# Optimization experiments

Hardware: AMD Instinct MI355X
Metric: run time of the kernel (lower is better)

Reference implementation:

```python
import jax, jax.numpy as jnp
import numpy as np

NUM_PRODUCTS = 100000
NUM_CATEGORIES = 1000
P_DIM = 64          # product embedding dim
C_DIM = P_DIM // 2  # 32
T_DIM = P_DIM // 4  # 16
U_DIM = P_DIM // 4  # 16
HID = 128
B, S, L = 1024, 50, 20


def setup_inputs() -> dict:
    key = jax.random.key(0)
    ks = jax.random.split(key, 24)
    inp = {}
    inp['product_input'] = jax.random.randint(ks[0], (B, S, L), 1, NUM_PRODUCTS + 1, dtype=jnp.int32)
    inp['categories_input'] = jax.random.randint(ks[1], (B, S, L), 1, NUM_CATEGORIES + 1, dtype=jnp.int32)
    inp['user_age_input'] = jax.random.uniform(ks[2], (B,), jnp.float32) * 80.0
    inp['user_timestamps_input'] = jax.random.uniform(ks[3], (B, S), jnp.float32)
    inp['user_gender_input'] = jax.random.randint(ks[4], (B,), 0, 2).astype(jnp.float32)
    # embedding tables (padding_idx=0 -> zero row)
    emb_p = jax.random.normal(ks[5], (NUM_PRODUCTS + 1, P_DIM), jnp.float32) * 0.02
    inp['emb_p'] = emb_p.at[0].set(0.0)
    emb_c = jax.random.normal(ks[6], (NUM_CATEGORIES + 1, C_DIM), jnp.float32) * 0.02
    inp['emb_c'] = emb_c.at[0].set(0.0)
    # small linears
    inp['W_ts'] = jax.random.normal(ks[7], (T_DIM, 1), jnp.float32) * 0.1
    inp['b_ts'] = jnp.zeros((T_DIM,), jnp.float32)
    inp['W_uf'] = jax.random.normal(ks[8], (U_DIM, 2), jnp.float32) * 0.1
    inp['b_uf'] = jnp.zeros((U_DIM,), jnp.float32)
    # 2-layer LSTM params (torch layout: [4H, in], gate order i,f,g,o)
    IN = P_DIM + C_DIM + T_DIM + U_DIM  # 128
    sc = 1.0 / np.sqrt(HID)
    inp['W_ih0'] = jax.random.uniform(ks[9], (4 * HID, IN), jnp.float32, -sc, sc)
    inp['W_hh0'] = jax.random.uniform(ks[10], (4 * HID, HID), jnp.float32, -sc, sc)
    inp['b_ih0'] = jax.random.uniform(ks[11], (4 * HID,), jnp.float32, -sc, sc)
    inp['b_hh0'] = jax.random.uniform(ks[12], (4 * HID,), jnp.float32, -sc, sc)
    inp['W_ih1'] = jax.random.uniform(ks[13], (4 * HID, HID), jnp.float32, -sc, sc)
    inp['W_hh1'] = jax.random.uniform(ks[14], (4 * HID, HID), jnp.float32, -sc, sc)
    inp['b_ih1'] = jax.random.uniform(ks[15], (4 * HID,), jnp.float32, -sc, sc)
    inp['b_hh1'] = jax.random.uniform(ks[16], (4 * HID,), jnp.float32, -sc, sc)
    # MLP head
    inp['W1'] = jax.random.normal(ks[17], (HID // 2, HID), jnp.float32) * 0.05
    inp['b1'] = jnp.zeros((HID // 2,), jnp.float32)
    inp['W2'] = jax.random.normal(ks[18], (NUM_PRODUCTS + 1, HID // 2), jnp.float32) * 0.05
    inp['b2'] = jnp.zeros((NUM_PRODUCTS + 1,), jnp.float32)
    return inp


def _lstm_layer(x, Wih, Whh, bih, bhh):
    # x: [S, B, D] -> outputs [S, B, H], final h [B, H]
    Bb = x.shape[1]
    h0 = jnp.zeros((Bb, HID), x.dtype)
    def step(carry, xt):
        h, c = carry
        gates = xt @ Wih.T + bih + h @ Whh.T + bhh
        i, f, g, o = jnp.split(gates, 4, axis=-1)
        c = jax.nn.sigmoid(f) * c + jax.nn.sigmoid(i) * jnp.tanh(g)
        h = jax.nn.sigmoid(o) * jnp.tanh(c)
        return (h, c), h
    (h, c), ys = jax.lax.scan(step, (h0, h0), x)
    return ys, h


def reference(product_input, categories_input, user_age_input, user_timestamps_input,
              user_gender_input, emb_p, emb_c, W_ts, b_ts, W_uf, b_uf,
              W_ih0, W_hh0, b_ih0, b_hh0, W_ih1, W_hh1, b_ih1, b_hh1,
              W1, b1, W2, b2):
    # per-basket mean-pooled embeddings (fused gather + segment mean)
    prod = emb_p[product_input].mean(axis=2)          # [B, S, 64]
    cat = emb_c[categories_input].mean(axis=2)        # [B, S, 32]
    ts = user_timestamps_input[..., None] @ W_ts.T + b_ts  # [B, S, 16]
    uf = jnp.stack([user_age_input, user_gender_input], axis=1) @ W_uf.T + b_uf  # [B, 16]
    uf = jnp.broadcast_to(uf[:, None, :], (uf.shape[0], prod.shape[1], uf.shape[1]))
    x = jnp.concatenate([prod, cat, ts, uf], axis=-1)  # [B, S, 128]
    x = jnp.transpose(x, (1, 0, 2))                    # [S, B, 128]
    ys0, _ = _lstm_layer(x, W_ih0, W_hh0, b_ih0, b_hh0)
    _, h_last = _lstm_layer(ys0, W_ih1, W_hh1, b_ih1, b_hh1)  # [B, H]
    # dropout is identity in eval mode
    hidden = jax.nn.relu(h_last @ W1.T + b1)
    logits = hidden @ W2.T + b2                        # [B, num_products+1]
    return logits
```

## Files before the change

kernel.cpp:

```cpp
#include <hip/hip_runtime.h>

#define B_    1024
#define S_    50
#define L_    20
#define NOUT  100001

typedef __attribute__((ext_vector_type(8))) short bh8;
typedef __attribute__((ext_vector_type(4))) float fx4;

__device__ __forceinline__ unsigned short f2bf(float x){
  unsigned u = __float_as_uint(x);
  unsigned r = (u + 0x7FFFu + ((u >> 16) & 1u)) >> 16;
  return (unsigned short)r;
}
__device__ __forceinline__ float bf2f(unsigned short h){
  return __uint_as_float(((unsigned)h) << 16);
}
__device__ __forceinline__ float sigm(float x){ return 1.f/(1.f + __expf(-x)); }
__device__ __forceinline__ float tanh_(float x){ return 1.f - 2.f/(__expf(2.f*x) + 1.f); }

__device__ __forceinline__ void frag_convert_row(const float* src, bh8& hv, bh8& lv){
  #pragma unroll
  for (int j = 0; j < 8; j++){
    float x = src[j];
    unsigned short hb = f2bf(x);
    hv[j] = (short)hb;
    lv[j] = (short)f2bf(x - bf2f(hb));
  }
}

__global__ __launch_bounds__(256) void prep_lstm_w(
    const float* __restrict__ Wih0, const float* __restrict__ Whh0,
    const float* __restrict__ bih0, const float* __restrict__ bhh0,
    const float* __restrict__ Wih1, const float* __restrict__ Whh1,
    const float* __restrict__ bih1, const float* __restrict__ bhh1,
    short* __restrict__ wsw, float* __restrict__ wsbias){
  int tid = blockIdx.x*256 + threadIdx.x;
  if (tid < 1024){
    int l = tid >> 9, n = tid & 511;
    wsbias[l*512 + n] = l ? (bih1[n] + bhh1[n]) : (bih0[n] + bhh0[n]);
  }
  if (tid >= 32768) return;
  int lane = tid & 63;
  int kt   = (tid >> 6) & 7;
  int nt   = (tid >> 9) & 31;
  int l    = tid >> 14;
  const float* Wih = l ? Wih1 : Wih0;
  const float* Whh = l ? Whh1 : Whh0;
  int n = nt*16 + (lane & 15);
  int kbase = kt*32 + (lane >> 4)*8;
  size_t base = ((((size_t)l*32 + nt)*8 + kt)*64 + lane)*8;
  for (int j = 0; j < 8; j++){
    int k = kbase + j;
    float w = (k < 128) ? Wih[n*128 + k] : Whh[n*128 + (k - 128)];
    wsw[base + j] = (short)f2bf(w);
  }
}

__global__ __launch_bounds__(256) void prep_w2(const float* __restrict__ W2,
                                               short* __restrict__ out){
  long i = (long)blockIdx.x*256 + threadIdx.x;
  if (i >= 100016L*64) return;
  long row = i >> 6;
  float v = (row < NOUT) ? W2[i] : 0.f;
  out[i] = (short)f2bf(v);
}

__global__ __launch_bounds__(256) void features(
    const int* __restrict__ pidx, const int* __restrict__ cidx,
    const float* __restrict__ age, const float* __restrict__ ts,
    const float* __restrict__ gender,
    const float* __restrict__ embp, const float* __restrict__ embc,
    const float* __restrict__ Wts, const float* __restrict__ bts,
    const float* __restrict__ Wuf, const float* __restrict__ bufv,
    short* __restrict__ xfrag){
  const int bx = blockIdx.x;
  const int bt = bx & 63, s = bx >> 6;
  const int b0 = bt*16;
  const int tid = threadIdx.x;
  __shared__ int pi[320], ci[320];
  __shared__ __align__(16) float XF[16][132];
  for (int i = tid; i < 640; i += 256){
    if (i < 320){
      int row = i/20, l = i - row*20;
      pi[i] = pidx[((size_t)(b0+row)*S_ + s)*L_ + l];
    } else {
      int j = i - 320;
      int row = j/20, l = j - row*20;
      ci[j] = cidx[((size_t)(b0+row)*S_ + s)*L_ + l];
    }
  }
  __syncthreads();
  const int m = tid >> 4, fg = tid & 15;
  float a[8];
  if (fg < 8){
    int f0 = fg*8;
    float4 s0 = {0,0,0,0}, s1 = {0,0,0,0};
    for (int l = 0; l < L_; l++){
      const float4* p = (const float4*)(embp + (size_t)pi[m*20+l]*64 + f0);
      float4 u = p[0], v = p[1];
      s0.x += u.x; s0.y += u.y; s0.z += u.z; s0.w += u.w;
      s1.x += v.x; s1.y += v.y; s1.z += v.z; s1.w += v.w;
    }
    a[0]=s0.x*0.05f; a[1]=s0.y*0.05f; a[2]=s0.z*0.05f; a[3]=s0.w*0.05f;
    a[4]=s1.x*0.05f; a[5]=s1.y*0.05f; a[6]=s1.z*0.05f; a[7]=s1.w*0.05f;
  } else if (fg < 12){
    int f0 = (fg-8)*8;
    float4 s0 = {0,0,0,0}, s1 = {0,0,0,0};
    for (int l = 0; l < L_; l++){
      const float4* p = (const float4*)(embc + (size_t)ci[m*20+l]*32 + f0);
      float4 u = p[0], v = p[1];
      s0.x += u.x; s0.y += u.y; s0.z += u.z; s0.w += u.w;
      s1.x += v.x; s1.y += v.y; s1.z += v.z; s1.w += v.w;
    }
    a[0]=s0.x*0.05f; a[1]=s0.y*0.05f; a[2]=s0.z*0.05f; a[3]=s0.w*0.05f;
    a[4]=s1.x*0.05f; a[5]=s1.y*0.05f; a[6]=s1.z*0.05f; a[7]=s1.w*0.05f;
  } else if (fg < 14){
    int j0 = (fg-12)*8;
    float tv = ts[(size_t)(b0+m)*S_ + s];
    #pragma unroll
    for (int e = 0; e < 8; e++) a[e] = tv*Wts[j0+e] + bts[j0+e];
  } else {
    int j0 = (fg-14)*8;
    float av = age[b0+m], gv = gender[b0+m];
    #pragma unroll
    for (int e = 0; e < 8; e++){
      int j = j0+e;
      a[e] = av*Wuf[2*j] + gv*Wuf[2*j+1] + bufv[j];
    }
  }
  {
    int f0 = fg*8;
    *(float4*)&XF[m][f0]   = (float4){a[0],a[1],a[2],a[3]};
    *(float4*)&XF[m][f0+4] = (float4){a[4],a[5],a[6],a[7]};
  }
  __syncthreads();
  const int kt = tid >> 6, ls = tid & 63;
  const int mm = ls & 15, a2 = ls >> 4;
  bh8 hv, lv;
  frag_convert_row(&XF[mm][kt*32 + a2*8], hv, lv);
  size_t ob = ((((size_t)s*64 + bt)*2 + 0)*4 + kt)*512 + (size_t)ls*8;
  *(bh8*)(xfrag + ob)        = hv;
  *(bh8*)(xfrag + ob + 2048) = lv;
}

__global__ __launch_bounds__(512, 2) void lstm_kernel(
    const short* __restrict__ xfrag, const short* __restrict__ wsw,
    const float* __restrict__ wsbias,
    const float* __restrict__ W1, const float* __restrict__ b1,
    short* __restrict__ hidden_bf){
  __shared__ __align__(16) short XA0hi[2][2048], XA0lo[2][2048];
  __shared__ __align__(16) short HA0hi[2048],   HA0lo[2048];
  __shared__ __align__(16) short A1hi[4096],    A1lo[4096];
  __shared__ __align__(16) float XHf[16][132];
  const int tid  = threadIdx.x;
  const int w    = tid >> 6, lane = tid & 63;
  const int col  = lane & 15, quad = lane >> 4;
  const int bt   = blockIdx.x;
  const int plane = tid >> 8, sl = tid & 255;
  const bh8* wp = (const bh8*)wsw;

  for (int i = tid; i < 2048; i += 512){
    HA0hi[i] = 0; HA0lo[i] = 0;
    A1hi[2048 + i] = 0; A1lo[2048 + i] = 0;
  }
  float bz[2][4];
  #pragma unroll
  for (int l = 0; l < 2; l++)
    #pragma unroll
    for (int g = 0; g < 4; g++)
      bz[l][g] = wsbias[l*512 + (g*8 + w)*16 + col];
  fx4 c0 = {0,0,0,0}, c1 = {0,0,0,0};
  {
    float4 v = *(const float4*)(xfrag + ((size_t)bt*2 + plane)*2048 + (size_t)sl*8);
    *(float4*)((plane ? XA0lo[0] : XA0hi[0]) + sl*8) = v;
  }

  for (int t = 0; t < S_; t++){
    __syncthreads();
    const int tb = t & 1;
    int tp = (t+1 < S_) ? t+1 : S_-1;
    float4 pf = *(const float4*)(xfrag + (((size_t)tp*64 + bt)*2 + plane)*2048 + (size_t)sl*8);

    fx4 acc[4];
    #pragma unroll
    for (int g = 0; g < 4; g++) acc[g] = (fx4){bz[0][g], bz[0][g], bz[0][g], bz[0][g]};
    #pragma unroll
    for (int kt = 0; kt < 8; kt++){
      const short* ph = (kt < 4) ? &XA0hi[tb][kt*512 + lane*8] : &HA0hi[(kt-4)*512 + lane*8];
      const short* pl = (kt < 4) ? &XA0lo[tb][kt*512 + lane*8] : &HA0lo[(kt-4)*512 + lane*8];
      bh8 ah = *(const bh8*)ph;
      bh8 al = *(const bh8*)pl;
      #pragma unroll
      for (int g = 0; g < 4; g++){
        bh8 bb = wp[(size_t)((g*8 + w)*8 + kt)*64 + lane];
        acc[g] = __builtin_amdgcn_mfma_f32_16x16x32_bf16(ah, bb, acc[g], 0, 0, 0);
        acc[g] = __builtin_amdgcn_mfma_f32_16x16x32_bf16(al, bb, acc[g], 0, 0, 0);
      }
    }
    #pragma unroll
    for (int r = 0; r < 4; r++){
      float cc = sigm(acc[1][r])*c0[r] + sigm(acc[0][r])*tanh_(acc[2][r]);
      c0[r] = cc;
      XHf[quad*4 + r][w*16 + col] = sigm(acc[3][r])*tanh_(cc);
    }
    __syncthreads();
    if (tid < 256){
      const int kt4 = tid >> 6, ls2 = tid & 63;
      const int mm = ls2 & 15, a2 = ls2 >> 4;
      bh8 hv, lv;
      frag_convert_row(&XHf[mm][kt4*32 + a2*8], hv, lv);
      *(bh8*)&A1hi[kt4*512 + ls2*8] = hv;
      *(bh8*)&A1lo[kt4*512 + ls2*8] = lv;
      *(bh8*)&HA0hi[kt4*512 + ls2*8] = hv;
      *(bh8*)&HA0lo[kt4*512 + ls2*8] = lv;
    }
    __syncthreads();

    #pragma unroll
    for (int g = 0; g < 4; g++) acc[g] = (fx4){bz[1][g], bz[1][g], bz[1][g], bz[1][g]};
    #pragma unroll
    for (int kt = 0; kt < 8; kt++){
      bh8 ah = *(const bh8*)&A1hi[kt*512 + lane*8];
      bh8 al = *(const bh8*)&A1lo[kt*512 + lane*8];
      #pragma unroll
      for (int g = 0; g < 4; g++){
        bh8 bb = wp[(size_t)((32 + g*8 + w)*8 + kt)*64 + lane];
        acc[g] = __builtin_amdgcn_mfma_f32_16x16x32_bf16(ah, bb, acc[g], 0, 0, 0);
        acc[g] = __builtin_amdgcn_mfma_f32_16x16x32_bf16(al, bb, acc[g], 0, 0, 0);
      }
    }
    *(float4*)((plane ? XA0lo[(t+1)&1] : XA0hi[(t+1)&1]) + sl*8) = pf;
    #pragma unroll
    for (int r = 0; r < 4; r++){
      float cc = sigm(acc[1][r])*c1[r] + sigm(acc[0][r])*tanh_(acc[2][r]);
      c1[r] = cc;
      XHf[quad*4 + r][w*16 + col] = sigm(acc[3][r])*tanh_(cc);
    }
    __syncthreads();
    if (tid < 256){
      const int kt4 = tid >> 6, ls2 = tid & 63;
      const int mm = ls2 & 15, a2 = ls2 >> 4;
      bh8 hv, lv;
      frag_convert_row(&XHf[mm][kt4*32 + a2*8], hv, lv);
      *(bh8*)&A1hi[(4+kt4)*512 + ls2*8] = hv;
      *(bh8*)&A1lo[(4+kt4)*512 + ls2*8] = lv;
    }
  }
  #pragma unroll
  for (int e = 0; e < 2; e++){
    int mm = (tid >> 6)*2 + e;
    int cc = tid & 63;
    float s = b1[cc];
    #pragma unroll 8
    for (int k = 0; k < 128; k++) s += XHf[mm][k]*W1[cc*128 + k];
    s = fmaxf(s, 0.f);
    hidden_bf[(size_t)(bt*16 + mm)*64 + cc] = (short)f2bf(s);
  }
}

__global__ __launch_bounds__(256) void head2(
    const short* __restrict__ hid, const short* __restrict__ w2,
    const float* __restrict__ b2, float* __restrict__ out){
  __shared__ __align__(16) float HS[4][16][132];
  const int tid = threadIdx.x;
  const int w = tid >> 6, lane = tid & 63;
  const int col = lane & 15, quad = lane >> 4;
  const int mt = blockIdx.x & 63;
  const int chunk = blockIdx.x >> 6;
  const bh8* hp = (const bh8*)hid;
  bh8 a0 = hp[(size_t)(mt*16 + col)*8 + quad];
  bh8 a1 = hp[(size_t)(mt*16 + col)*8 + 4 + quad];
  const bh8* wpt = (const bh8*)w2;
  #pragma unroll
  for (int i = 0; i < 8; i++){
    int nt = chunk*32 + w*8 + i;
    if (nt < 6251){
      int n = nt*16 + col;
      bh8 b0v = wpt[(size_t)n*8 + quad];
      bh8 b1v = wpt[(size_t)n*8 + 4 + quad];
      fx4 a = {0.f,0.f,0.f,0.f};
      a = __builtin_amdgcn_mfma_f32_16x16x32_bf16(a0, b0v, a, 0, 0, 0);
      a = __builtin_amdgcn_mfma_f32_16x16x32_bf16(a1, b1v, a, 0, 0, 0);
      float bias = (n < NOUT) ? b2[n] : 0.f;
      #pragma unroll
      for (int r = 0; r < 4; r++) HS[w][quad*4 + r][i*16 + col] = a[r] + bias;
    }
  }
  __syncthreads();
  const long rowbase = (long)mt*16;
  const int n0 = chunk*512 + w*128;
  #pragma unroll
  for (int p = 0; p < 8; p++){
    int row = p*2 + (lane >> 5);
    int c4 = (lane & 31)*4;
    int gc = n0 + c4;
    float4 v = *(const float4*)&HS[w][row][c4];
    if (gc + 3 < NOUT){
      *(float4*)&out[(rowbase + row)*NOUT + gc] = v;
    } else {
      float vv[4] = {v.x, v.y, v.z, v.w};
      #pragma unroll
      for (int k2 = 0; k2 < 4; k2++)
        if (gc + k2 < NOUT) out[(rowbase + row)*NOUT + gc + k2] = vv[k2];
    }
  }
}

extern "C" void kernel_launch(void* const* d_in, const int* in_sizes, int n_in,
                              void* d_out, int out_size, void* d_ws, size_t ws_size,
                              hipStream_t stream){
  const int*   prod = (const int*)  d_in[0];
  const int*   cat  = (const int*)  d_in[1];
  const float* age  = (const float*)d_in[2];
  const float* ts   = (const float*)d_in[3];
  const float* gen  = (const float*)d_in[4];
  const float* embp = (const float*)d_in[5];
  const float* embc = (const float*)d_in[6];
  const float* Wts  = (const float*)d_in[7];
  const float* bts  = (const float*)d_in[8];
  const float* Wuf  = (const float*)d_in[9];
  const float* bufv = (const float*)d_in[10];
  const float* Wih0 = (const float*)d_in[11];
  const float* Whh0 = (const float*)d_in[12];
  const float* bih0 = (const float*)d_in[13];
  const float* bhh0 = (const float*)d_in[14];
  const float* Wih1 = (const float*)d_in[15];
  const float* Whh1 = (const float*)d_in[16];
  const float* bih1 = (const float*)d_in[17];
  const float* bhh1 = (const float*)d_in[18];
  const float* W1   = (const float*)d_in[19];
  const float* b1   = (const float*)d_in[20];
  const float* W2   = (const float*)d_in[21];
  const float* b2   = (const float*)d_in[22];
  float* out = (float*)d_out;

  char* ws = (char*)d_ws;
  short* ws_x    = (short*)(ws);
  short* ws_w    = (short*)(ws + 26214400);
  float* ws_bias = (float*)(ws + 26738688);
  short* ws_hid  = (short*)(ws + 26742784);
  short* ws_w2   = (short*)(ws + 26873856);

  prep_lstm_w<<<128, 256, 0, stream>>>(Wih0, Whh0, bih0, bhh0,
                                       Wih1, Whh1, bih1, bhh1, ws_w, ws_bias);
  prep_w2<<<25004, 256, 0, stream>>>(W2, ws_w2);
  features<<<3200, 256, 0, stream>>>(prod, cat, age, ts, gen, embp, embc,
                                     Wts, bts, Wuf, bufv, ws_x);
  lstm_kernel<<<64, 512, 0, stream>>>(ws_x, ws_w, ws_bias, W1, b1, ws_hid);
  head2<<<196*64, 256, 0, stream>>>(ws_hid, ws_w2, b2, out);
}
```

Before: 1.139 ms.

## Wavefront-pipeline the two LSTM layers across warp groups with one barrier per step

The LSTM kernel now puts layer 0 on warps 0-3 and layer 1 on warps 4-7. Layer 1 runs one timestep behind layer 0, using double-buffered hidden-state tiles, so both layers compute in the same iteration with a single __syncthreads per step instead of four. Each warp covers two column tiles per gate, and every warp does its own hi/lo bf16 fragment conversion, replacing the half-block conversion phase. Sigmoid and tanh now use the hardware reciprocal instead of a division, which is slightly less accurate.

```diff
diff --git a/kernel.cpp b/kernel.cpp
--- a/kernel.cpp
+++ b/kernel.cpp
@@ -16,8 +16,12 @@
 __device__ __forceinline__ float bf2f(unsigned short h){
   return __uint_as_float(((unsigned)h) << 16);
 }
-__device__ __forceinline__ float sigm(float x){ return 1.f/(1.f + __expf(-x)); }
-__device__ __forceinline__ float tanh_(float x){ return 1.f - 2.f/(__expf(2.f*x) + 1.f); }
+__device__ __forceinline__ float sigm(float x){
+  return __builtin_amdgcn_rcpf(1.f + __expf(-x));
+}
+__device__ __forceinline__ float tanh_(float x){
+  return 1.f - 2.f*__builtin_amdgcn_rcpf(__expf(2.f*x) + 1.f);
+}
 
 __device__ __forceinline__ void frag_convert_row(const float* src, bh8& hv, bh8& lv){
   #pragma unroll
@@ -149,113 +153,106 @@
     const float* __restrict__ wsbias,
     const float* __restrict__ W1, const float* __restrict__ b1,
     short* __restrict__ hidden_bf){
-  __shared__ __align__(16) short XA0hi[2][2048], XA0lo[2][2048];
-  __shared__ __align__(16) short HA0hi[2048],   HA0lo[2048];
-  __shared__ __align__(16) short A1hi[4096],    A1lo[4096];
-  __shared__ __align__(16) float XHf[16][132];
+  __shared__ __align__(16) short XAhi[2][2048], XAlo[2][2048];
+  __shared__ __align__(16) short H0hi[2][2048], H0lo[2][2048];
+  __shared__ __align__(16) short H1hi[2][2048], H1lo[2][2048];
+  __shared__ __align__(16) float XH0f[16][132], XH1f[16][132];
   const int tid  = threadIdx.x;
   const int w    = tid >> 6, lane = tid & 63;
   const int col  = lane & 15, quad = lane >> 4;
   const int bt   = blockIdx.x;
+  const int u    = w & 3;
+  const bool t1  = (w >= 4);
+  const int lsel = t1 ? 1 : 0;
   const int plane = tid >> 8, sl = tid & 255;
   const bh8* wp = (const bh8*)wsw;
 
-  for (int i = tid; i < 2048; i += 512){
-    HA0hi[i] = 0; HA0lo[i] = 0;
-    A1hi[2048 + i] = 0; A1lo[2048 + i] = 0;
+  for (int idx = tid; idx < 2048; idx += 512){
+    H0hi[1][idx] = 0; H0lo[1][idx] = 0;
+    H1hi[0][idx] = 0; H1lo[0][idx] = 0;
   }
   float bz[2][4];
   #pragma unroll
-  for (int l = 0; l < 2; l++)
+  for (int ss = 0; ss < 2; ss++)
     #pragma unroll
     for (int g = 0; g < 4; g++)
-      bz[l][g] = wsbias[l*512 + (g*8 + w)*16 + col];
-  fx4 c0 = {0,0,0,0}, c1 = {0,0,0,0};
+      bz[ss][g] = wsbias[lsel*512 + (g*8 + 2*u + ss)*16 + col];
+  float cst[2][4] = {{0,0,0,0},{0,0,0,0}};
   {
     float4 v = *(const float4*)(xfrag + ((size_t)bt*2 + plane)*2048 + (size_t)sl*8);
-    *(float4*)((plane ? XA0lo[0] : XA0hi[0]) + sl*8) = v;
-  }
-
-  for (int t = 0; t < S_; t++){
+    *(float4*)((plane ? XAlo[0] : XAhi[0]) + sl*8) = v;
+  }
+  __syncthreads();
+
+  for (int i = 0; i <= S_; i++){
+    const int cb = i & 1, pb = cb ^ 1;
+    int tp = (i+1 < S_) ? i+1 : S_-1;
+    float4 pf = *(const float4*)(xfrag + (((size_t)tp*64 + bt)*2 + plane)*2048 + (size_t)sl*8);
+
+    const bool act = t1 ? (i >= 1) : (i < S_);
+    if (act){
+      fx4 acc[2][4];
+      #pragma unroll
+      for (int ss = 0; ss < 2; ss++)
+        #pragma unroll
+        for (int g = 0; g < 4; g++)
+          acc[ss][g] = (fx4){bz[ss][g], bz[ss][g], bz[ss][g], bz[ss][g]};
+      #pragma unroll
+      for (int kt = 0; kt < 8; kt++){
+        const short* ph;
+        const short* pl;
+        if (!t1){
+          ph = (kt < 4) ? &XAhi[cb][kt*512 + lane*8] : &H0hi[pb][(kt-4)*512 + lane*8];
+          pl = (kt < 4) ? &XAlo[cb][kt*512 + lane*8] : &H0lo[pb][(kt-4)*512 + lane*8];
+        } else {
+          ph = (kt < 4) ? &H0hi[pb][kt*512 + lane*8] : &H1hi[pb][(kt-4)*512 + lane*8];
+          pl = (kt < 4) ? &H0lo[pb][kt*512 + lane*8] : &H1lo[pb][(kt-4)*512 + lane*8];
+        }
+        bh8 ah = *(const bh8*)ph;
+        bh8 al = *(const bh8*)pl;
+        #pragma unroll
+        for (int ss = 0; ss < 2; ss++)
+          #pragma unroll
+          for (int g = 0; g < 4; g++){
+            bh8 bb = wp[(size_t)((lsel*32 + g*8 + 2*u + ss)*8 + kt)*64 + lane];
+            acc[ss][g] = __builtin_amdgcn_mfma_f32_16x16x32_bf16(ah, bb, acc[ss][g], 0, 0, 0);
+            acc[ss][g] = __builtin_amdgcn_mfma_f32_16x16x32_bf16(al, bb, acc[ss][g], 0, 0, 0);
+          }
+      }
+      float (*XH)[132] = t1 ? XH1f : XH0f;
+      #pragma unroll
+      for (int ss = 0; ss < 2; ss++)
+        #pragma unroll
+        for (int r = 0; r < 4; r++){
+          float cc = sigm(acc[ss][1][r])*cst[ss][r] + sigm(acc[ss][0][r])*tanh_(acc[ss][2][r]);
+          cst[ss][r] = cc;
+          XH[quad*4 + r][u*32 + ss*16 + col] = sigm(acc[ss][3][r])*tanh_(cc);
+        }
+      {
+        const int mm = lane & 15, a2 = lane >> 4;
+        bh8 hv, lv;
+        frag_convert_row(&XH[mm][u*32 + a2*8], hv, lv);
+        if (!t1){
+          *(bh8*)&H0hi[cb][u*512 + lane*8] = hv;
+          *(bh8*)&H0lo[cb][u*512 + lane*8] = lv;
+        } else {
+          *(bh8*)&H1hi[cb][u*512 + lane*8] = hv;
+          *(bh8*)&H1lo[cb][u*512 + lane*8] = lv;
+        }
+      }
+    }
+    *(float4*)((plane ? XAlo[pb] : XAhi[pb]) + sl*8) = pf;
     __syncthreads();
-    const int tb = t & 1;
-    int tp = (t+1 < S_) ? t+1 : S_-1;
-    float4 pf = *(const float4*)(xfrag + (((size_t)tp*64 + bt)*2 + plane)*2048 + (size_t)sl*8);
-
-    fx4 acc[4];
-    #pragma unroll
-    for (int g = 0; g < 4; g++) acc[g] = (fx4){bz[0][g], bz[0][g], bz[0][g], bz[0][g]};
-    #pragma unroll
-    for (int kt = 0; kt < 8; kt++){
-      const short* ph = (kt < 4) ? &XA0hi[tb][kt*512 + lane*8] : &HA0hi[(kt-4)*512 + lane*8];
-      const short* pl = (kt < 4) ? &XA0lo[tb][kt*512 + lane*8] : &HA0lo[(kt-4)*512 + lane*8];
-      bh8 ah = *(const bh8*)ph;
-      bh8 al = *(const bh8*)pl;
-      #pragma unroll
-      for (int g = 0; g < 4; g++){
-        bh8 bb = wp[(size_t)((g*8 + w)*8 + kt)*64 + lane];
-        acc[g] = __builtin_amdgcn_mfma_f32_16x16x32_bf16(ah, bb, acc[g], 0, 0, 0);
-        acc[g] = __builtin_amdgcn_mfma_f32_16x16x32_bf16(al, bb, acc[g], 0, 0, 0);
-      }
-    }
-    #pragma unroll
-    for (int r = 0; r < 4; r++){
-      float cc = sigm(acc[1][r])*c0[r] + sigm(acc[0][r])*tanh_(acc[2][r]);
-      c0[r] = cc;
-      XHf[quad*4 + r][w*16 + col] = sigm(acc[3][r])*tanh_(cc);
-    }
-    __syncthreads();
-    if (tid < 256){
-      const int kt4 = tid >> 6, ls2 = tid & 63;
-      const int mm = ls2 & 15, a2 = ls2 >> 4;
-      bh8 hv, lv;
-      frag_convert_row(&XHf[mm][kt4*32 + a2*8], hv, lv);
-      *(bh8*)&A1hi[kt4*512 + ls2*8] = hv;
-      *(bh8*)&A1lo[kt4*512 + ls2*8] = lv;
-      *(bh8*)&HA0hi[kt4*512 + ls2*8] = hv;
-      *(bh8*)&HA0lo[kt4*512 + ls2*8] = lv;
-    }
-    __syncthreads();
-
-    #pragma unroll
-    for (int g = 0; g < 4; g++) acc[g] = (fx4){bz[1][g], bz[1][g], bz[1][g], bz[1][g]};
-    #pragma unroll
-    for (int kt = 0; kt < 8; kt++){
-      bh8 ah = *(const bh8*)&A1hi[kt*512 + lane*8];
-      bh8 al = *(const bh8*)&A1lo[kt*512 + lane*8];
-      #pragma unroll
-      for (int g = 0; g < 4; g++){
-        bh8 bb = wp[(size_t)((32 + g*8 + w)*8 + kt)*64 + lane];
-        acc[g] = __builtin_amdgcn_mfma_f32_16x16x32_bf16(ah, bb, acc[g], 0, 0, 0);
-        acc[g] = __builtin_amdgcn_mfma_f32_16x16x32_bf16(al, bb, acc[g], 0, 0, 0);
-      }
-    }
-    *(float4*)((plane ? XA0lo[(t+1)&1] : XA0hi[(t+1)&1]) + sl*8) = pf;
-    #pragma unroll
-    for (int r = 0; r < 4; r++){
-      float cc = sigm(acc[1][r])*c1[r] + sigm(acc[0][r])*tanh_(acc[2][r]);
-      c1[r] = cc;
-      XHf[quad*4 + r][w*16 + col] = sigm(acc[3][r])*tanh_(cc);
-    }
-    __syncthreads();
-    if (tid < 256){
-      const int kt4 = tid >> 6, ls2 = tid & 63;
-      const int mm = ls2 & 15, a2 = ls2 >> 4;
-      bh8 hv, lv;
-      frag_convert_row(&XHf[mm][kt4*32 + a2*8], hv, lv);
-      *(bh8*)&A1hi[(4+kt4)*512 + ls2*8] = hv;
-      *(bh8*)&A1lo[(4+kt4)*512 + ls2*8] = lv;
-    }
   }
   #pragma unroll
   for (int e = 0; e < 2; e++){
-    int mm = (tid >> 6)*2 + e;
-    int cc = tid & 63;
-    float s = b1[cc];
+    int mm2 = (tid >> 6)*2 + e;
+    int cc2 = tid & 63;
+    float s = b1[cc2];
     #pragma unroll 8
-    for (int k = 0; k < 128; k++) s += XHf[mm][k]*W1[cc*128 + k];
+    for (int k = 0; k < 128; k++) s += XH1f[mm2][k]*W1[cc2*128 + k];
     s = fmaxf(s, 0.f);
-    hidden_bf[(size_t)(bt*16 + mm)*64 + cc] = (short)f2bf(s);
+    hidden_bf[(size_t)(bt*16 + mm2)*64 + cc2] = (short)f2bf(s);
   }
 }
 
```

New measurement: 1.097 ms. 3.7% less time.
